# Kernel optimization log

Hardware: AMD Instinct MI355X
Metric: run time of the kernel (lower is better)

The kernel has to match this reference:

```python
import jax, jax.numpy as jnp
import numpy as np
import math

MAX_K = 8
MAX_LEN = 128
ITER = 3
GAMMA = 2
NEG = -2.0**16 + 1.0  # mask fill value from torch code


def _squash(x):
    # NOTE: faithful to source: norm taken over axis=1 (capsule axis), keepdim
    sq = jnp.sum(x * x, axis=1, keepdims=True)
    return sq / (1.0 + sq) / jnp.sqrt(sq + 1e-9) * x


def _routing(low, B_mat, S):
    # low: [B, n, d] mailbox; B_mat: [1, MAX_K, MAX_LEN]; S: [d, d]
    n = low.shape[1]
    K_c = max(1, min(MAX_K, int(math.log2(n))))  # static per edge type
    low_new = jnp.einsum('bnd,de->bne', low, S)  # loop-invariant in torch too
    B_c = B_mat[:, :K_c, :]
    mask = jnp.arange(MAX_LEN) < n  # padded-neighbor mask
    high = None
    for _ in range(ITER):
        logits = jnp.where(mask, B_c, NEG)              # [1,K_c,L]
        W = jax.nn.softmax(logits, axis=-1)[:, :, :n]   # weights identical over batch
        high = _squash(jnp.einsum('xkn,bnd->bkd', W, low_new))
        delta = jnp.einsum('bkd,bnd->kn', high, low_new)  # batch-summed agreement
        B_c = B_c.at[0, :, :n].add(delta)  # padded cols get zero delta (zeros in low)
    high = jnp.pad(high, ((0, 0), (0, MAX_K - K_c), (0, 0)))
    # torch B_matrix_c aliases B_matrix; write slice back so next etype sees updates
    return high, B_mat.at[:, :K_c, :].set(B_c)


def setup_inputs() -> dict:
    key = jax.random.key(0)
    ks = jax.random.split(key, 12)
    d = 64
    n_user, n_rev, n_tag, n_rev_dst = 10000, 30000, 40000, 8000
    f = lambda k, s: jax.random.normal(k, s, dtype=jnp.float32)
    return {
        'review_embed': f(ks[0], (n_rev, d)),
        'tag_embed': f(ks[1], (n_tag, d)),
        'idx_urt': jax.random.randint(ks[2], (n_user, 64), 0, n_rev, dtype=jnp.int32),
        'idx_uqt': jax.random.randint(ks[3], (n_user, 32), 0, n_tag, dtype=jnp.int32),
        'idx_uprt': jax.random.randint(ks[4], (n_user, 50), 0, n_rev, dtype=jnp.int32),
        'idx_rht': jax.random.randint(ks[5], (n_rev_dst, 20), 0, n_tag, dtype=jnp.int32),
        'B_matrix': f(ks[6], (1, MAX_K, MAX_LEN)),
        'S_matrix': f(ks[7], (d, d)),
        'M1': f(ks[8], (d, d)),
        'M2': f(ks[9], (d, 1)),
    }


def reference(review_embed, tag_embed, idx_urt, idx_uqt, idx_uprt, idx_rht,
              B_matrix, S_matrix, M1, M2):
    # capsule routing per edge type, B_matrix threaded sequentially (torch aliasing)
    h_urt, B_matrix = _routing(review_embed[idx_urt], B_matrix, S_matrix)
    h_uqt, B_matrix = _routing(tag_embed[idx_uqt], B_matrix, S_matrix)
    h_uprt, B_matrix = _routing(review_embed[idx_uprt], B_matrix, S_matrix)
    all_u = jnp.concatenate([h_urt, h_uqt, h_uprt], axis=1)  # [B, 3*MAX_K, d]
    s = jnp.einsum('bkd,do->bko', jnp.tanh(jnp.einsum('bkd,de->bke', all_u, M1)), M2)[..., 0]
    s = s ** GAMMA
    att = jax.nn.softmax(s, axis=1)                # [B, 3*MAX_K]
    user_out = jnp.einsum('bk,bkd->bd', att, all_u)
    review_out = jnp.mean(tag_embed[idx_rht], axis=1)  # flag==2 mean reduce (r_h_t)
    return user_out, review_out
```

## Files before the change

### kernel.cpp

```cpp
#include <hip/hip_runtime.h>

#define NU 10000
#define NREV_DST 8000
#define MAIN_BLOCKS 512
#define TW (MAIN_BLOCKS * 4)
#define UPW ((NU + TW - 1) / TW)


template <int N, int K>
__global__ __launch_bounds__(256) void main_iter(
    const float* __restrict__ emb, const int* __restrict__ idx,
    const float* __restrict__ Sg, const float* __restrict__ Wg,
    float* __restrict__ delta_acc, float* __restrict__ allu,
    int slot0, int write_high, int write_delta)
{
    constexpr int NC = (N + 31) / 32;
    constexpr int P  = NC * 32;

    __shared__ float s_S[64 * 65];
    __shared__ float s_emb[4][32 * 65];
    __shared__ float s_g[4][K * 64];
    __shared__ float s_h[4][K * 64];

    const int tid  = threadIdx.x;
    const int w    = tid >> 6;
    const int lane = tid & 63;
    const int gw   = blockIdx.x * 4 + w;

    for (int i = tid; i < 64 * 64; i += 256) {
        s_S[(i >> 6) * 65 + (i & 63)] = Sg[i];
    }
    __syncthreads();

    float dreg[NC][K];
#pragma unroll
    for (int c = 0; c < NC; ++c)
#pragma unroll
        for (int k = 0; k < K; ++k) dreg[c][k] = 0.f;

    auto stage = [&](int u, int c, int m) {
        const int npass = (m + 3) >> 2;
        for (int p = 0; p < npass; ++p) {
            const int r = p * 4 + (lane >> 4);
            if (r < m) {
                const int row = idx[u * N + c * 32 + r];
                const float4 v =
                    *reinterpret_cast<const float4*>(emb + (size_t)row * 64 + (lane & 15) * 4);
                float* dst = &s_emb[w][r * 65 + (lane & 15) * 4];
                dst[0] = v.x; dst[1] = v.y; dst[2] = v.z; dst[3] = v.w;
            }
        }
    };

    for (int it = 0; it < UPW; ++it) {
        const int u = gw + it * TW;
        if (u < NU) {
            float g[K];
#pragma unroll
            for (int k = 0; k < K; ++k) g[k] = 0.f;
#pragma unroll
            for (int c = 0; c < NC; ++c) {
                const int m = (N - c * 32 < 32) ? (N - c * 32) : 32;
                stage(u, c, m);
                for (int r = 0; r < m; ++r) {
                    const float ev = s_emb[w][r * 65 + lane];
#pragma unroll
                    for (int k = 0; k < K; ++k)
                        g[k] = fmaf(Wg[k * 64 + c * 32 + r], ev, g[k]);
                }
            }
#pragma unroll
            for (int k = 0; k < K; ++k) s_g[w][k * 64 + lane] = g[k];
            float raw[K];
#pragma unroll
            for (int k = 0; k < K; ++k) raw[k] = 0.f;
            for (int e = 0; e < 64; ++e) {
                const float sv = s_S[e * 65 + lane];
#pragma unroll
                for (int k = 0; k < K; ++k) raw[k] = fmaf(s_g[w][k * 64 + e], sv, raw[k]);
            }
            float sq = 0.f;
#pragma unroll
            for (int k = 0; k < K; ++k) sq = fmaf(raw[k], raw[k], sq);
            const float f = (sq / (1.0f + sq)) / sqrtf(sq + 1e-9f);
            float hi[K];
#pragma unroll
            for (int k = 0; k < K; ++k) hi[k] = f * raw[k];
            if (write_high) {
#pragma unroll
                for (int k = 0; k < K; ++k)
                    allu[(size_t)u * 1024 + (slot0 + k) * 64 + lane] = hi[k];
            }
            if (write_delta) {
#pragma unroll
                for (int k = 0; k < K; ++k) s_h[w][k * 64 + lane] = hi[k];
                float hs[K];
#pragma unroll
                for (int k = 0; k < K; ++k) hs[k] = 0.f;
                for (int d = 0; d < 64; ++d) {
                    const float sv = s_S[lane * 65 + d];
#pragma unroll
                    for (int k = 0; k < K; ++k) hs[k] = fmaf(s_h[w][k * 64 + d], sv, hs[k]);
                }
#pragma unroll
                for (int k = 0; k < K; ++k) s_g[w][k * 64 + lane] = hs[k];
                const int nl = lane & 31, h = lane >> 5;
#pragma unroll
                for (int cc = NC - 1; cc >= 0; --cc) {
                    const int m = (N - cc * 32 < 32) ? (N - cc * 32) : 32;
                    if (cc != NC - 1) stage(u, cc, m);
                    if (nl < m) {
                        for (int eh = 0; eh < 32; ++eh) {
                            const int e = h * 32 + eh;
                            const float ev = s_emb[w][nl * 65 + e];
#pragma unroll
                            for (int k = 0; k < K; ++k)
                                dreg[cc][k] = fmaf(ev, s_g[w][k * 64 + e], dreg[cc][k]);
                        }
                    }
                }
            }
        }
    }

    if (write_delta) {
        __syncthreads();
        float* red = &s_emb[w][0];
        const int nl = lane & 31;
#pragma unroll
        for (int cc = 0; cc < NC; ++cc) {
#pragma unroll
            for (int k = 0; k < K; ++k) {
                const float v = dreg[cc][k] + __shfl_xor(dreg[cc][k], 32, 64);
                if (lane < 32) red[k * P + cc * 32 + nl] = v;
            }
        }
        __syncthreads();
        for (int t = tid; t < K * P; t += 256) {
            const float s = s_emb[0][t] + s_emb[1][t] + s_emb[2][t] + s_emb[3][t];
            const int k = t / P, n = t % P;
            atomicAdd(&delta_acc[k * 64 + n], s);
        }
    }
}

__global__ __launch_bounds__(1024) void update_kernel(
    float* __restrict__ Bstate, float* __restrict__ delta_acc,
    const float* __restrict__ Bin, float* __restrict__ Wout,
    int init, int Kc, int nc, int Kn, int nn)
{
    __shared__ float sB[1024];
    const int t = threadIdx.x;
    float b = init ? Bin[t] : Bstate[t];
    const int k = t >> 7, n = t & 127;
    float d = 0.f;
    if (!init && k < Kc && n < nc) d = delta_acc[k * 64 + n];
    __syncthreads();
    if (t < 512) delta_acc[t] = 0.f;
    b += d;
    Bstate[t] = b;
    sB[t] = b;
    __syncthreads();
    const int wv = t >> 6, lane = t & 63;
    if (wv < Kn) {
        float v = (lane < nn) ? sB[wv * 128 + lane] : -3.4e38f;
        float m = v;
#pragma unroll
        for (int off = 32; off >= 1; off >>= 1) m = fmaxf(m, __shfl_xor(m, off, 64));
        const float e = (lane < nn) ? expf(v - m) : 0.f;
        float s = e;
#pragma unroll
        for (int off = 32; off >= 1; off >>= 1) s += __shfl_xor(s, off, 64);
        Wout[wv * 64 + lane] = e / s;
    }
}

__global__ __launch_bounds__(256) void attn_kernel(
    const float* __restrict__ allu, const float* __restrict__ M1g,
    const float* __restrict__ M2g, float* __restrict__ out)
{
    __shared__ float sM1[64 * 65];
    __shared__ float sU[4][16 * 64];
    const int tid = threadIdx.x, w = tid >> 6, lane = tid & 63;
    for (int i = tid; i < 4096; i += 256)
        sM1[(i >> 6) * 65 + (i & 63)] = M1g[i];
    __syncthreads();
    const int u = blockIdx.x * 4 + w;
    if (u >= NU) return;
    for (int i = 0; i < 16; ++i)
        sU[w][i * 64 + lane] = allu[(size_t)u * 1024 + i * 64 + lane];
    const float m2 = M2g[lane];
    float acc[16];
#pragma unroll
    for (int i = 0; i < 16; ++i) acc[i] = 0.f;
    for (int d = 0; d < 64; ++d) {
        const float m1v = sM1[d * 65 + lane];
#pragma unroll
        for (int i = 0; i < 16; ++i) acc[i] = fmaf(sU[w][i * 64 + d], m1v, acc[i]);
    }
    float s2[16];
#pragma unroll
    for (int i = 0; i < 16; ++i) {
        float c = tanhf(acc[i]) * m2;
#pragma unroll
        for (int off = 32; off >= 1; off >>= 1) c += __shfl_xor(c, off, 64);
        s2[i] = c * c;
    }
    float mx = 0.f;
#pragma unroll
    for (int i = 0; i < 16; ++i) mx = fmaxf(mx, s2[i]);
    float den = 8.f * expf(-mx);
    float att[16];
#pragma unroll
    for (int i = 0; i < 16; ++i) { att[i] = expf(s2[i] - mx); den += att[i]; }
    const float inv = 1.0f / den;
    float o = 0.f;
#pragma unroll
    for (int i = 0; i < 16; ++i) o = fmaf(att[i] * inv, sU[w][i * 64 + lane], o);
    out[(size_t)u * 64 + lane] = o;
}

__global__ __launch_bounds__(256) void review_kernel(
    const float* __restrict__ tag, const int* __restrict__ idx, float* __restrict__ out)
{
    const int tid = threadIdx.x, w = tid >> 6, lane = tid & 63;
    const int r = blockIdx.x * 4 + w;
    if (r >= NREV_DST) return;
    float acc = 0.f;
    for (int j = 0; j < 20; ++j) {
        const int t = idx[r * 20 + j];
        acc += tag[(size_t)t * 64 + lane];
    }
    out[(size_t)r * 64 + lane] = acc / 20.0f;
}

extern "C" void kernel_launch(void* const* d_in, const int* in_sizes, int n_in,
                              void* d_out, int out_size, void* d_ws, size_t ws_size,
                              hipStream_t stream)
{
    const float* review_embed = (const float*)d_in[0];
    const float* tag_embed    = (const float*)d_in[1];
    const int*   idx_urt      = (const int*)d_in[2];
    const int*   idx_uqt      = (const int*)d_in[3];
    const int*   idx_uprt     = (const int*)d_in[4];
    const int*   idx_rht      = (const int*)d_in[5];
    const float* B_in         = (const float*)d_in[6];
    const float* S_g          = (const float*)d_in[7];
    const float* M1           = (const float*)d_in[8];
    const float* M2           = (const float*)d_in[9];

    float* ws     = (float*)d_ws;
    float* Bstate = ws;
    float* delta  = ws + 1024;
    float* Wbuf   = ws + 1536;
    float* allu   = ws + 2048;
    float* out    = (float*)d_out;

    const dim3 mg(MAIN_BLOCKS), mb(256);
    const dim3 one(1), ub(1024);

    hipLaunchKernelGGL(update_kernel, one, ub, 0, stream,
                       Bstate, delta, B_in, Wbuf, 1, 0, 0, 6, 64);

    for (int itr = 0; itr < 3; ++itr) {
        hipLaunchKernelGGL((main_iter<64, 6>), mg, mb, 0, stream,
                           review_embed, idx_urt, S_g, Wbuf, delta, allu,
                           0, (itr == 2) ? 1 : 0, 1);
        const int Kn = (itr == 2) ? 5 : 6;
        const int nn = (itr == 2) ? 32 : 64;
        hipLaunchKernelGGL(update_kernel, one, ub, 0, stream,
                           Bstate, delta, B_in, Wbuf, 0, 6, 64, Kn, nn);
    }
    for (int itr = 0; itr < 3; ++itr) {
        hipLaunchKernelGGL((main_iter<32, 5>), mg, mb, 0, stream,
                           tag_embed, idx_uqt, S_g, Wbuf, delta, allu,
                           6, (itr == 2) ? 1 : 0, 1);
        const int nn = (itr == 2) ? 50 : 32;
        hipLaunchKernelGGL(update_kernel, one, ub, 0, stream,
                           Bstate, delta, B_in, Wbuf, 0, 5, 32, 5, nn);
    }
    for (int itr = 0; itr < 3; ++itr) {
        const int last = (itr == 2);
        hipLaunchKernelGGL((main_iter<50, 5>), mg, mb, 0, stream,
                           review_embed, idx_uprt, S_g, Wbuf, delta, allu,
                           11, last, last ? 0 : 1);
        if (!last)
            hipLaunchKernelGGL(update_kernel, one, ub, 0, stream,
                               Bstate, delta, B_in, Wbuf, 0, 5, 50, 5, 50);
    }

    hipLaunchKernelGGL(attn_kernel, dim3((NU + 3) / 4), mb, 0, stream, allu, M1, M2, out);
    hipLaunchKernelGGL(review_kernel, dim3((NREV_DST + 3) / 4), mb, 0, stream,
                       tag_embed, idx_rht, out + (size_t)NU * 64);
}
```

Before: 665.3 us.

## Map one user per wave, use readlane broadcasts and swizzled shared S

The main routing kernel launches 2500 blocks so each wave handles exactly one user instead of looping over users, and adds an occupancy hint to launch bounds. The per-lane matrix products now broadcast the per-lane g/hi/hs values with readlane instead of staging them through shared memory. S is stored with an XOR swizzle so the transposed reads avoid bank conflicts without padding. The embedding gather for the delta step goes through a small transposed tile, and W is written k-minor so its loads coalesce. These changes aim to cut LDS traffic and barriers and raise occupancy, at the cost of many more blocks each issuing delta atomics.

```diff
diff --git a/kernel.cpp b/kernel.cpp
--- a/kernel.cpp
+++ b/kernel.cpp
@@ -2,144 +2,156 @@
 
 #define NU 10000
 #define NREV_DST 8000
-#define MAIN_BLOCKS 512
-#define TW (MAIN_BLOCKS * 4)
-#define UPW ((NU + TW - 1) / TW)
-
+#define MAIN_BLOCKS 2500
+
+
+__device__ __forceinline__ float rlane(float v, int l) {
+    return __int_as_float(__builtin_amdgcn_readlane(__float_as_int(v), l));
+}
 
 template <int N, int K>
-__global__ __launch_bounds__(256) void main_iter(
+__global__ __launch_bounds__(256, 4) void main_iter(
     const float* __restrict__ emb, const int* __restrict__ idx,
     const float* __restrict__ Sg, const float* __restrict__ Wg,
     float* __restrict__ delta_acc, float* __restrict__ allu,
     int slot0, int write_high, int write_delta)
 {
-    constexpr int NC = (N + 31) / 32;
-    constexpr int P  = NC * 32;
-
-    __shared__ float s_S[64 * 65];
-    __shared__ float s_emb[4][32 * 65];
-    __shared__ float s_g[4][K * 64];
-    __shared__ float s_h[4][K * 64];
+    __shared__ float s_S[64 * 64];
+    __shared__ float s_embT[4][64 * 20];
 
     const int tid  = threadIdx.x;
     const int w    = tid >> 6;
     const int lane = tid & 63;
-    const int gw   = blockIdx.x * 4 + w;
 
     for (int i = tid; i < 64 * 64; i += 256) {
-        s_S[(i >> 6) * 65 + (i & 63)] = Sg[i];
+        const int r = i >> 6, c = i & 63;
+        s_S[r * 64 + ((((c >> 2) ^ (r & 15)) << 2) | (c & 3))] = Sg[i];
     }
     __syncthreads();
 
-    float dreg[NC][K];
-#pragma unroll
-    for (int c = 0; c < NC; ++c)
-#pragma unroll
-        for (int k = 0; k < K; ++k) dreg[c][k] = 0.f;
-
-    auto stage = [&](int u, int c, int m) {
-        const int npass = (m + 3) >> 2;
-        for (int p = 0; p < npass; ++p) {
-            const int r = p * 4 + (lane >> 4);
-            if (r < m) {
-                const int row = idx[u * N + c * 32 + r];
-                const float4 v =
-                    *reinterpret_cast<const float4*>(emb + (size_t)row * 64 + (lane & 15) * 4);
-                float* dst = &s_emb[w][r * 65 + (lane & 15) * 4];
-                dst[0] = v.x; dst[1] = v.y; dst[2] = v.z; dst[3] = v.w;
-            }
-        }
-    };
-
-    for (int it = 0; it < UPW; ++it) {
-        const int u = gw + it * TW;
-        if (u < NU) {
-            float g[K];
-#pragma unroll
-            for (int k = 0; k < K; ++k) g[k] = 0.f;
-#pragma unroll
-            for (int c = 0; c < NC; ++c) {
-                const int m = (N - c * 32 < 32) ? (N - c * 32) : 32;
-                stage(u, c, m);
-                for (int r = 0; r < m; ++r) {
-                    const float ev = s_emb[w][r * 65 + lane];
-#pragma unroll
-                    for (int k = 0; k < K; ++k)
-                        g[k] = fmaf(Wg[k * 64 + c * 32 + r], ev, g[k]);
+    const int u = __builtin_amdgcn_readfirstlane((int)blockIdx.x * 4 + w);
+    const int* uidx = idx + u * N;
+
+    float g[K];
+#pragma unroll
+    for (int k = 0; k < K; ++k) g[k] = 0.f;
+#pragma unroll
+    for (int r0 = 0; r0 < N; r0 += 8) {
+        float ev[8];
+#pragma unroll
+        for (int i = 0; i < 8; ++i)
+            if (r0 + i < N) {
+                const int row = uidx[r0 + i];
+                ev[i] = emb[(size_t)row * 64 + lane];
+            }
+#pragma unroll
+        for (int i = 0; i < 8; ++i)
+            if (r0 + i < N) {
+#pragma unroll
+                for (int k = 0; k < K; ++k)
+                    g[k] = fmaf(Wg[(r0 + i) * 8 + k], ev[i], g[k]);
+            }
+    }
+
+    float raw[K];
+#pragma unroll
+    for (int k = 0; k < K; ++k) raw[k] = 0.f;
+    {
+        const int l4 = lane >> 2, lo = lane & 3;
+#pragma unroll 4
+        for (int eo = 0; eo < 16; ++eo) {
+            const int a = eo * 64 + (((l4 ^ eo) << 2) | lo);
+            const float sv0 = s_S[a];
+            const float sv1 = s_S[a + 16 * 64];
+            const float sv2 = s_S[a + 32 * 64];
+            const float sv3 = s_S[a + 48 * 64];
+#pragma unroll
+            for (int k = 0; k < K; ++k) {
+                raw[k] = fmaf(rlane(g[k], eo),      sv0, raw[k]);
+                raw[k] = fmaf(rlane(g[k], eo + 16), sv1, raw[k]);
+                raw[k] = fmaf(rlane(g[k], eo + 32), sv2, raw[k]);
+                raw[k] = fmaf(rlane(g[k], eo + 48), sv3, raw[k]);
+            }
+        }
+    }
+
+    float sq = 0.f;
+#pragma unroll
+    for (int k = 0; k < K; ++k) sq = fmaf(raw[k], raw[k], sq);
+    const float f = (sq / (1.0f + sq)) / sqrtf(sq + 1e-9f);
+    float hi[K];
+#pragma unroll
+    for (int k = 0; k < K; ++k) hi[k] = f * raw[k];
+
+    if (write_high) {
+#pragma unroll
+        for (int k = 0; k < K; ++k)
+            allu[(size_t)u * 1024 + (slot0 + k) * 64 + lane] = hi[k];
+    }
+
+    if (write_delta) {
+        float hs[K];
+#pragma unroll
+        for (int k = 0; k < K; ++k) hs[k] = 0.f;
+        {
+            const int rowbase = lane * 64, l15 = lane & 15;
+#pragma unroll 4
+            for (int d4 = 0; d4 < 16; ++d4) {
+                const float4 sv = *(const float4*)&s_S[rowbase + ((d4 ^ l15) << 2)];
+#pragma unroll
+                for (int k = 0; k < K; ++k) {
+                    hs[k] = fmaf(rlane(hi[k], d4 * 4 + 0), sv.x, hs[k]);
+                    hs[k] = fmaf(rlane(hi[k], d4 * 4 + 1), sv.y, hs[k]);
+                    hs[k] = fmaf(rlane(hi[k], d4 * 4 + 2), sv.z, hs[k]);
+                    hs[k] = fmaf(rlane(hi[k], d4 * 4 + 3), sv.w, hs[k]);
                 }
             }
-#pragma unroll
-            for (int k = 0; k < K; ++k) s_g[w][k * 64 + lane] = g[k];
-            float raw[K];
-#pragma unroll
-            for (int k = 0; k < K; ++k) raw[k] = 0.f;
-            for (int e = 0; e < 64; ++e) {
-                const float sv = s_S[e * 65 + lane];
-#pragma unroll
-                for (int k = 0; k < K; ++k) raw[k] = fmaf(s_g[w][k * 64 + e], sv, raw[k]);
-            }
-            float sq = 0.f;
-#pragma unroll
-            for (int k = 0; k < K; ++k) sq = fmaf(raw[k], raw[k], sq);
-            const float f = (sq / (1.0f + sq)) / sqrtf(sq + 1e-9f);
-            float hi[K];
-#pragma unroll
-            for (int k = 0; k < K; ++k) hi[k] = f * raw[k];
-            if (write_high) {
-#pragma unroll
-                for (int k = 0; k < K; ++k)
-                    allu[(size_t)u * 1024 + (slot0 + k) * 64 + lane] = hi[k];
-            }
-            if (write_delta) {
-#pragma unroll
-                for (int k = 0; k < K; ++k) s_h[w][k * 64 + lane] = hi[k];
-                float hs[K];
-#pragma unroll
-                for (int k = 0; k < K; ++k) hs[k] = 0.f;
-                for (int d = 0; d < 64; ++d) {
-                    const float sv = s_S[lane * 65 + d];
-#pragma unroll
-                    for (int k = 0; k < K; ++k) hs[k] = fmaf(s_h[w][k * 64 + d], sv, hs[k]);
+        }
+
+        float dreg[K];
+#pragma unroll
+        for (int k = 0; k < K; ++k) dreg[k] = 0.f;
+
+        constexpr int RP = (N + 15) / 16;
+        const int rr = lane >> 2, jj = lane & 3;
+        int rows[RP];
+#pragma unroll
+        for (int p = 0; p < RP; ++p) {
+            const int r = p * 16 + rr;
+            rows[p] = (N % 16 == 0 || r < N) ? uidx[r] : 0;
+        }
+
+        for (int ec = 0; ec < 4; ++ec) {
+            const int e0 = ec * 16;
+#pragma unroll
+            for (int p = 0; p < RP; ++p) {
+                const int r = p * 16 + rr;
+                if (N % 16 == 0 || r < N) {
+                    const float4 v =
+                        *(const float4*)(emb + (size_t)rows[p] * 64 + e0 + jj * 4);
+                    *(float4*)&s_embT[w][r * 20 + jj * 4] = v;
                 }
-#pragma unroll
-                for (int k = 0; k < K; ++k) s_g[w][k * 64 + lane] = hs[k];
-                const int nl = lane & 31, h = lane >> 5;
-#pragma unroll
-                for (int cc = NC - 1; cc >= 0; --cc) {
-                    const int m = (N - cc * 32 < 32) ? (N - cc * 32) : 32;
-                    if (cc != NC - 1) stage(u, cc, m);
-                    if (nl < m) {
-                        for (int eh = 0; eh < 32; ++eh) {
-                            const int e = h * 32 + eh;
-                            const float ev = s_emb[w][nl * 65 + e];
-#pragma unroll
-                            for (int k = 0; k < K; ++k)
-                                dreg[cc][k] = fmaf(ev, s_g[w][k * 64 + e], dreg[cc][k]);
-                        }
-                    }
+            }
+#pragma unroll
+            for (int e4 = 0; e4 < 4; ++e4) {
+                const float4 v = *(const float4*)&s_embT[w][lane * 20 + e4 * 4];
+                const int e = e0 + e4 * 4;
+#pragma unroll
+                for (int k = 0; k < K; ++k) {
+                    dreg[k] = fmaf(v.x, rlane(hs[k], e + 0), dreg[k]);
+                    dreg[k] = fmaf(v.y, rlane(hs[k], e + 1), dreg[k]);
+                    dreg[k] = fmaf(v.z, rlane(hs[k], e + 2), dreg[k]);
+                    dreg[k] = fmaf(v.w, rlane(hs[k], e + 3), dreg[k]);
                 }
             }
         }
-    }
-
-    if (write_delta) {
+
+#pragma unroll
+        for (int k = 0; k < K; ++k) s_embT[w][k * 64 + lane] = dreg[k];
         __syncthreads();
-        float* red = &s_emb[w][0];
-        const int nl = lane & 31;
-#pragma unroll
-        for (int cc = 0; cc < NC; ++cc) {
-#pragma unroll
-            for (int k = 0; k < K; ++k) {
-                const float v = dreg[cc][k] + __shfl_xor(dreg[cc][k], 32, 64);
-                if (lane < 32) red[k * P + cc * 32 + nl] = v;
-            }
-        }
-        __syncthreads();
-        for (int t = tid; t < K * P; t += 256) {
-            const float s = s_emb[0][t] + s_emb[1][t] + s_emb[2][t] + s_emb[3][t];
-            const int k = t / P, n = t % P;
-            atomicAdd(&delta_acc[k * 64 + n], s);
+        for (int t = tid; t < K * 64; t += 256) {
+            const float s = s_embT[0][t] + s_embT[1][t] + s_embT[2][t] + s_embT[3][t];
+            if ((t & 63) < N) atomicAdd(&delta_acc[t], s);
         }
     }
 }
@@ -171,7 +183,7 @@
         float s = e;
 #pragma unroll
         for (int off = 32; off >= 1; off >>= 1) s += __shfl_xor(s, off, 64);
-        Wout[wv * 64 + lane] = e / s;
+        Wout[lane * 8 + wv] = e / s;
     }
 }
 
```

After: 793.3 us. 1.19x slower.
